# Kernel tuning notes

Hardware: AMD Instinct MI355X
Metric: run time of the kernel (lower is better)

The kernel has to match this reference:

```python
import jax, jax.numpy as jnp
import numpy as np

B, S, H = 2, 4096, 2048
NH, NKV, HD = 16, 4, 128          # heads, kv heads, head_dim = H // NH
GS_RATIO = 0.25                    # hardcoded in MyAttention.forward
ROPE_BASE = 10000.0


def rotate_half(x):
    h = x.shape[-1] // 2
    return jnp.concatenate((-x[..., h:], x[..., :h]), axis=-1)


def setup_inputs() -> dict:
    key = jax.random.key(0)
    ks = jax.random.split(key, 5)
    g = int(S * GS_RATIO)
    hidden_states = jax.random.normal(ks[0], (B, S, H), jnp.float32)
    position_ids = jnp.tile(jnp.arange(S, dtype=jnp.int32)[None, :], (B, 1))
    # causal additive mask per group window (0 keep, -1e9 masked)
    i = jnp.arange(g)
    causal = i[None, :] <= i[:, None]
    attention_mask = jnp.broadcast_to(
        jnp.where(causal, 0.0, -1e9).astype(jnp.float32)[None, None], (B, 1, g, g)
    )
    sc = 0.02
    Wq = (jax.random.normal(ks[1], (H, NH * HD), jnp.float32) * sc)
    Wk = (jax.random.normal(ks[2], (H, NKV * HD), jnp.float32) * sc)
    Wv = (jax.random.normal(ks[3], (H, NKV * HD), jnp.float32) * sc)
    Wo = (jax.random.normal(ks[4], (NH * HD, H), jnp.float32) * sc)
    return {"hidden_states": hidden_states, "attention_mask": attention_mask,
            "position_ids": position_ids, "Wq": Wq, "Wk": Wk, "Wv": Wv, "Wo": Wo}


def reference(hidden_states, attention_mask, position_ids, Wq, Wk, Wv, Wo):
    B_, S_, H_ = hidden_states.shape
    g = int(S_ * GS_RATIO)
    ng = S_ // g
    n_rep = NH // NKV

    # QKV projections -> (B, heads, S, HD)
    q = (hidden_states @ Wq).reshape(B_, S_, NH, HD).transpose(0, 2, 1, 3)
    k = (hidden_states @ Wk).reshape(B_, S_, NKV, HD).transpose(0, 2, 1, 3)
    v = (hidden_states @ Wv).reshape(B_, S_, NKV, HD).transpose(0, 2, 1, 3)

    # RoPE
    inv_freq = 1.0 / (ROPE_BASE ** (jnp.arange(0, HD, 2, dtype=jnp.float32) / HD))
    t = jnp.arange(S_, dtype=jnp.float32)
    emb = jnp.concatenate([jnp.outer(t, inv_freq)] * 2, axis=-1)  # (S, HD)
    cos = jnp.cos(emb)[position_ids][:, None]  # (B,1,S,HD)
    sin = jnp.sin(emb)[position_ids][:, None]
    q = q * cos + rotate_half(q) * sin
    k = k * cos + rotate_half(k) * sin

    # GQA repeat_kv
    k = jnp.repeat(k, n_rep, axis=1)
    v = jnp.repeat(v, n_rep, axis=1)

    # S2-Attn shift: roll second half of heads by -g/2 along seq, then group
    def shift(x):
        x = jnp.concatenate([x[:, :NH // 2],
                             jnp.roll(x[:, NH // 2:], -g // 2, axis=2)], axis=1)
        return x.transpose(0, 2, 1, 3).reshape(B_ * ng, g, NH, HD).transpose(0, 2, 1, 3)

    q, k, v = shift(q), shift(k), shift(v)

    attn = jnp.einsum('bhqd,bhkd->bhqk', q, k) / np.float32(np.sqrt(HD))
    mask = jnp.tile(attention_mask, (ng, 1, 1, 1))  # (B*ng,1,g,g)
    attn = attn + mask
    attn = jax.nn.softmax(attn.astype(jnp.float32), axis=-1).astype(q.dtype)

    out = jnp.einsum('bhqk,bhkd->bhqd', attn, v)  # (B*ng, NH, g, HD)
    out = out.transpose(0, 2, 1, 3).reshape(B_, S_, NH, HD)
    # undo shift for second half of heads (+g/2 along seq)
    out = jnp.concatenate([out[:, :, :NH // 2],
                           jnp.roll(out[:, :, NH // 2:], g // 2, axis=1)], axis=2)
    out = out.reshape(B_, S_, NH * HD) @ Wo
    return out
```

## Files before the change

kernel.cpp:

```cpp
#include <hip/hip_runtime.h>
#include <math.h>

typedef unsigned short u16;
typedef short bf16x8 __attribute__((ext_vector_type(8)));
typedef float f32x4 __attribute__((ext_vector_type(4)));


__device__ __forceinline__ u16 f2bf(float x) {
  union { float f; unsigned u; } c; c.f = x;
  unsigned r = (c.u + 0x7FFFu + ((c.u >> 16) & 1u)) >> 16;
  return (u16)r;
}
__device__ __forceinline__ float bf2f(u16 x) {
  union { unsigned u; float f; } c; c.u = ((unsigned)x) << 16;
  return c.f;
}

#define GLD16(gp, lp)                                                   \
  __builtin_amdgcn_global_load_lds(                                     \
      (__attribute__((address_space(1))) void*)(gp),                    \
      (__attribute__((address_space(3))) void*)(lp), 16, 0, 0)

__global__ __launch_bounds__(256) void cast_bf16_vec(
    const float* __restrict__ X, u16* __restrict__ Y) {
  const size_t i = ((size_t)blockIdx.x * 256 + threadIdx.x) * 4;
  float4 v = *(const float4*)(X + i);
  ushort4 o;
  o.x = f2bf(v.x); o.y = f2bf(v.y); o.z = f2bf(v.z); o.w = f2bf(v.w);
  *(ushort4*)(Y + i) = o;
}

__global__ __launch_bounds__(256) void wt_cast(
    const float* __restrict__ W, u16* __restrict__ Wt, int K, int N) {
  const int bk = blockIdx.y * 64;
  const int bn = blockIdx.x * 64;
  __shared__ float T[64 * 65];
  const int tid = threadIdx.x;
  #pragma unroll
  for (int u = 0; u < 16; ++u) {
    int idx = tid + u * 256;
    int kl = idx >> 6, nl = idx & 63;
    T[kl * 65 + nl] = W[(size_t)(bk + kl) * N + bn + nl];
  }
  __syncthreads();
  #pragma unroll
  for (int u = 0; u < 16; ++u) {
    int idx = tid + u * 256;
    int nl = idx >> 6, kl = idx & 63;
    Wt[(size_t)(bn + nl) * K + bk + kl] = f2bf(T[kl * 65 + nl]);
  }
}

__global__ __launch_bounds__(512) void gemm_bf16_256(
    const u16* __restrict__ A, const u16* __restrict__ Bt,
    float* __restrict__ Cf, u16* __restrict__ Cb, int M, int N, int K) {
  __shared__ u16 As[4][256 * 32];
  __shared__ u16 Bs[4][256 * 32];

  const int tid = threadIdx.x;

  const int gridN = N >> 8;
  const int nwg = gridDim.x * gridDim.y;
  const int orig = blockIdx.y * gridDim.x + blockIdx.x;
  const int q8 = nwg >> 3, r8 = nwg & 7;
  const int xcd = orig & 7, lid = orig >> 3;
  const int wgid = (xcd < r8 ? xcd * (q8 + 1) : r8 * (q8 + 1) + (xcd - r8) * q8) + lid;
  const int bm = (wgid / gridN) << 8;
  const int bn = (wgid % gridN) << 8;

  const int w = tid >> 6, lane = tid & 63;
  const int col = lane & 15, quad = lane >> 4;
  const int wm = w >> 2, wn = w & 3;
  const int sw = (col >> 1) & 3;

  const int srow = tid >> 2;
  const int scp  = tid & 3;
  const int sc   = scp ^ ((srow >> 1) & 3);

  const u16* Ag = A  + (size_t)bm * K;
  const u16* Bg = Bt + (size_t)bn * K;
  const u16* aS0 = Ag + (size_t)srow * K + sc * 8;
  const u16* aS1 = Ag + (size_t)(srow + 128) * K + sc * 8;
  const u16* bS0 = Bg + (size_t)srow * K + sc * 8;
  const u16* bS1 = Bg + (size_t)(srow + 128) * K + sc * 8;
  const int ldst0 = srow * 32 + scp * 8;
  const int ldst1 = (srow + 128) * 32 + scp * 8;

#define STAGE_A(t, buf) { GLD16(aS0 + (size_t)(t) * 32, &As[buf][ldst0]); \
                          GLD16(aS1 + (size_t)(t) * 32, &As[buf][ldst1]); }
#define STAGE_B(t, buf) { GLD16(bS0 + (size_t)(t) * 32, &Bs[buf][ldst0]); \
                          GLD16(bS1 + (size_t)(t) * 32, &Bs[buf][ldst1]); }

  f32x4 acc[8][4];
  #pragma unroll
  for (int i = 0; i < 8; ++i)
    #pragma unroll
    for (int j = 0; j < 4; ++j) acc[i][j] = (f32x4)(0.0f);

  const int NT = K >> 5;

  STAGE_A(0, 0); STAGE_B(0, 0);
  if (NT > 1) {
    STAGE_A(1, 1); STAGE_B(1, 1);
    asm volatile("s_waitcnt vmcnt(4)" ::: "memory");
  } else {
    asm volatile("s_waitcnt vmcnt(0)" ::: "memory");
  }
  __builtin_amdgcn_s_barrier();
  asm volatile("" ::: "memory");

  const int aoff = (wm * 128 + col) * 32 + (quad ^ sw) * 8;
  const int boff = (wn * 64  + col) * 32 + (quad ^ sw) * 8;

  for (int t = 0; t < NT; ++t) {
    const int cur = t & 3;
    const bool pf = (t + 2 < NT);
    const int pbuf = (t + 2) & 3;

    bf16x8 af[4], bfr[4];
    #pragma unroll
    for (int i = 0; i < 4; ++i)
      af[i] = *(const bf16x8*)&As[cur][aoff + (16 * i) * 32];
    #pragma unroll
    for (int j = 0; j < 4; ++j)
      bfr[j] = *(const bf16x8*)&Bs[cur][boff + (16 * j) * 32];
    if (pf) STAGE_A(t + 2, pbuf);
    __builtin_amdgcn_s_barrier();
    asm volatile("s_waitcnt lgkmcnt(0)");
    __builtin_amdgcn_s_setprio(1);
    #pragma unroll
    for (int i = 0; i < 4; ++i)
      #pragma unroll
      for (int j = 0; j < 4; ++j)
        acc[i][j] = __builtin_amdgcn_mfma_f32_16x16x32_bf16(af[i], bfr[j], acc[i][j], 0, 0, 0);
    __builtin_amdgcn_s_setprio(0);
    __builtin_amdgcn_s_barrier();

    bf16x8 af2[4];
    #pragma unroll
    for (int i = 0; i < 4; ++i)
      af2[i] = *(const bf16x8*)&As[cur][aoff + ((64 + 16 * i)) * 32];
    if (pf) STAGE_B(t + 2, pbuf);
    __builtin_amdgcn_s_barrier();
    asm volatile("s_waitcnt lgkmcnt(0)");
    __builtin_amdgcn_s_setprio(1);
    #pragma unroll
    for (int i = 0; i < 4; ++i)
      #pragma unroll
      for (int j = 0; j < 4; ++j)
        acc[4 + i][j] = __builtin_amdgcn_mfma_f32_16x16x32_bf16(af2[i], bfr[j], acc[4 + i][j], 0, 0, 0);
    __builtin_amdgcn_s_setprio(0);

    if (pf) asm volatile("s_waitcnt vmcnt(4)" ::: "memory");
    else    asm volatile("s_waitcnt vmcnt(0)" ::: "memory");
    __builtin_amdgcn_s_barrier();
    asm volatile("" ::: "memory");
  }

  const int crow0 = bm + wm * 128 + quad * 4;
  const int ccol0 = bn + wn * 64 + col;
  #pragma unroll
  for (int i = 0; i < 8; ++i) {
    const int row0 = crow0 + 16 * i;
    #pragma unroll
    for (int j = 0; j < 4; ++j) {
      const int cc = ccol0 + 16 * j;
      #pragma unroll
      for (int r = 0; r < 4; ++r) {
        if (Cb) Cb[(size_t)(row0 + r) * N + cc] = f2bf(acc[i][j][r]);
        else    Cf[(size_t)(row0 + r) * N + cc] = acc[i][j][r];
      }
    }
  }
#undef STAGE_A
#undef STAGE_B
}

__global__ __launch_bounds__(256) void rope_qkv(
    u16* __restrict__ QKV, const int* __restrict__ pos) {
  const unsigned idx = blockIdx.x * 256 + threadIdx.x;
  const int d = idx & 63;
  const unsigned rest = idx >> 6;
  const int hh = rest % 20;
  const unsigned bs = rest / 20;

  const int colbase = (hh < 16) ? hh * 128 : 2048 + (hh - 16) * 128;
  u16* p = QKV + (size_t)bs * 3072 + colbase + d;
  const float x0 = bf2f(p[0]);
  const float x1 = bf2f(p[64]);
  const float t = (float)pos[bs];
  const float inv_freq = __expf((float)d * -0.14391156509676332f);
  float s, c;
  __sincosf(t * inv_freq, &s, &c);
  const float sc = (hh < 16) ? 0.08838834764831845f : 1.0f;
  p[0]  = f2bf((x0 * c - x1 * s) * sc);
  p[64] = f2bf((x1 * c + x0 * s) * sc);
}

__global__ __launch_bounds__(256) void v_transpose(
    const u16* __restrict__ QKV, u16* __restrict__ Vt) {
  const int bid = blockIdx.x;
  const int st = bid & 63;
  const int kvh = (bid >> 6) & 3;
  const int b = bid >> 8;
  __shared__ u16 T[64 * 136];
  const int tid = threadIdx.x;
  #pragma unroll
  for (int u = 0; u < 4; ++u) {
    int idx = tid + u * 256;
    int sl = idx >> 4, ch = idx & 15;
    *(uint4*)&T[sl * 136 + ch * 8] =
        *(const uint4*)(QKV + ((size_t)(b * 4096 + st * 64 + sl)) * 3072 + 2560 + kvh * 128 + ch * 8);
  }
  __syncthreads();
  #pragma unroll
  for (int u = 0; u < 32; ++u) {
    int idx = tid + u * 256;
    int d = idx >> 6, sl = idx & 63;
    Vt[((size_t)((b * 4 + kvh) * 128 + d)) * 4096 + st * 64 + sl] = T[sl * 136 + d];
  }
}

__global__ __launch_bounds__(256) void attn_mfma(
    const u16* __restrict__ QKV, const u16* __restrict__ Vt,
    u16* __restrict__ Ob) {
  __shared__ u16 Ks[2][64 * 128];
  __shared__ u16 Vs[2][128 * 64];
  __shared__ u16 Ps[4][16 * 72];

  const int bid = blockIdx.x;
  const int qt = 15 - (bid & 15);
  const int h  = (bid >> 4) & 15;
  const int gi = (bid >> 8) & 3;
  const int b  = bid >> 10;

  const int tid = threadIdx.x;
  const int w = tid >> 6, lane = tid & 63;
  const int col = lane & 15, quad = lane >> 4;

  const int shift = (h >= 8) ? 512 : 0;
  const int base_s = gi * 1024;
  const int kvh = h >> 2;

  const int kco8 = ((tid & 15) ^ ((tid >> 4) & 7)) << 3;
  const int vco8 = ((tid & 7) ^ ((tid >> 3) & 7)) << 3;
  const size_t krow = (size_t)(tid >> 4) * 3072 + kco8;
  const size_t vrow = (size_t)(tid >> 3) * 4096 + vco8;
  u16* kdst = &Ks[0][0] + tid * 8;
  u16* vdst = &Vs[0][0] + tid * 8;
  const size_t vbase = (size_t)((b * 4 + kvh) * 128) * 4096;
  const u16* kgb = QKV + (size_t)b * 4096 * 3072 + 2048 + kvh * 128;

#define ASTAGE(kt_, buf_) {                                               \
    const int sk_ = (base_s + (kt_) * 64 + shift) & 4095;                 \
    const u16* ks_ = kgb + (size_t)sk_ * 3072;                            \
    const u16* vs_ = Vt + vbase + sk_;                                    \
    GLD16(ks_ + krow,             kdst + (buf_) * 8192);                  \
    GLD16(ks_ + krow + 16 * 3072, kdst + (buf_) * 8192 + 2048);           \
    GLD16(ks_ + krow + 32 * 3072, kdst + (buf_) * 8192 + 4096);           \
    GLD16(ks_ + krow + 48 * 3072, kdst + (buf_) * 8192 + 6144);           \
    GLD16(vs_ + vrow,             vdst + (buf_) * 8192);                  \
    GLD16(vs_ + vrow + 32 * 4096, vdst + (buf_) * 8192 + 2048);           \
    GLD16(vs_ + vrow + 64 * 4096, vdst + (buf_) * 8192 + 4096);           \
    GLD16(vs_ + vrow + 96 * 4096, vdst + (buf_) * 8192 + 6144);           \
  }

  const int sq0 = (base_s + qt * 64 + shift) & 4095;
  {
    const u16* qsrc = QKV + ((size_t)(b * 4096 + sq0)) * 3072 + h * 128;
    GLD16(qsrc + krow,             kdst);
    GLD16(qsrc + krow + 16 * 3072, kdst + 2048);
    GLD16(qsrc + krow + 32 * 3072, kdst + 4096);
    GLD16(qsrc + krow + 48 * 3072, kdst + 6144);
  }
  asm volatile("s_waitcnt vmcnt(0)" ::: "memory");
  __builtin_amdgcn_s_barrier();
  asm volatile("" ::: "memory");

  const int cxor = col & 7;
  bf16x8 aq[4];
  {
    const int qr = w * 16 + col;
    #pragma unroll
    for (int kk = 0; kk < 4; ++kk)
      aq[kk] = *(const bf16x8*)&Ks[0][qr * 128 + ((((kk << 2) + quad) ^ cxor) << 3)];
  }
  asm volatile("s_waitcnt lgkmcnt(0)" ::: "memory");
  __builtin_amdgcn_s_barrier();
  asm volatile("" ::: "memory");

  ASTAGE(0, 0);

  f32x4 o[8];
  #pragma unroll
  for (int jd = 0; jd < 8; ++jd) o[jd] = (f32x4)(0.0f);
  float lp[4] = {0.0f, 0.0f, 0.0f, 0.0f};

  u16* Pw = &Ps[w][0];
  const int qrow_l = w * 16 + quad * 4;

  for (int kt = 0; kt <= qt; ++kt) {
    const u16* Kc = &Ks[kt & 1][0];
    const u16* Vc = &Vs[kt & 1][0];
    const bool pf = (kt < qt);
    if (pf) ASTAGE(kt + 1, (kt + 1) & 1);
    if (pf) asm volatile("s_waitcnt vmcnt(8)" ::: "memory");
    else    asm volatile("s_waitcnt vmcnt(0)" ::: "memory");
    __builtin_amdgcn_s_barrier();
    asm volatile("" ::: "memory");

    f32x4 scv[4];
    #pragma unroll
    for (int j = 0; j < 4; ++j) scv[j] = (f32x4)(0.0f);
    __builtin_amdgcn_s_setprio(1);
    #pragma unroll
    for (int kk = 0; kk < 4; ++kk) {
      #pragma unroll
      for (int j = 0; j < 4; ++j) {
        bf16x8 bk = *(const bf16x8*)&Kc[(16 * j + col) * 128 + ((((kk << 2) + quad) ^ cxor) << 3)];
        scv[j] = __builtin_amdgcn_mfma_f32_16x16x32_bf16(aq[kk], bk, scv[j], 0, 0, 0);
      }
    }
    __builtin_amdgcn_s_setprio(0);

    const bool last = (kt == qt);
    #pragma unroll
    for (int j = 0; j < 4; ++j) {
      #pragma unroll
      for (int r = 0; r < 4; ++r) {
        float p = __expf(scv[j][r]);
        if (last && (16 * j + col) > (qrow_l + r)) p = 0.0f;
        lp[r] += p;
        Pw[(quad * 4 + r) * 72 + 16 * j + col] = f2bf(p);
      }
    }

    __builtin_amdgcn_s_setprio(1);
    #pragma unroll
    for (int ks = 0; ks < 2; ++ks) {
      bf16x8 ap = *(const bf16x8*)&Pw[col * 72 + ks * 32 + quad * 8];
      #pragma unroll
      for (int jd = 0; jd < 8; ++jd) {
        bf16x8 bv = *(const bf16x8*)&Vc[(16 * jd + col) * 64 + ((((ks << 2) + quad) ^ cxor) << 3)];
        o[jd] = __builtin_amdgcn_mfma_f32_16x16x32_bf16(ap, bv, o[jd], 0, 0, 0);
      }
    }
    __builtin_amdgcn_s_setprio(0);

    asm volatile("" ::: "memory");
    __builtin_amdgcn_s_barrier();
  }
#undef ASTAGE

  #pragma unroll
  for (int r = 0; r < 4; ++r) {
    lp[r] += __shfl_xor(lp[r], 1, 64);
    lp[r] += __shfl_xor(lp[r], 2, 64);
    lp[r] += __shfl_xor(lp[r], 4, 64);
    lp[r] += __shfl_xor(lp[r], 8, 64);
  }

  #pragma unroll
  for (int r = 0; r < 4; ++r) {
    const int qg = qt * 64 + w * 16 + quad * 4 + r;
    const int sq = (base_s + qg + shift) & 4095;
    u16* dst = Ob + ((size_t)(b * 4096 + sq)) * 2048 + h * 128;
    const float inv = 1.0f / lp[r];
    #pragma unroll
    for (int jd = 0; jd < 8; ++jd)
      dst[16 * jd + col] = f2bf(o[jd][r] * inv);
  }
}

extern "C" void kernel_launch(void* const* d_in, const int* in_sizes, int n_in,
                              void* d_out, int out_size, void* d_ws, size_t ws_size,
                              hipStream_t stream) {
  const float* hs = (const float*)d_in[0];
  const int*   pos = (const int*)d_in[2];
  const float* Wq = (const float*)d_in[3];
  const float* Wk = (const float*)d_in[4];
  const float* Wv = (const float*)d_in[5];
  const float* Wo = (const float*)d_in[6];

  char* ws = (char*)d_ws;
  u16* hsb   = (u16*)ws; ws += (size_t)8192 * 2048 * 2;
  u16* Wqkvt = (u16*)ws; ws += (size_t)3072 * 2048 * 2;
  u16* Wot   = (u16*)ws; ws += (size_t)2048 * 2048 * 2;
  u16* QKVb  = (u16*)ws; ws += (size_t)8192 * 3072 * 2;
  u16* Vtt   = (u16*)ws; ws += (size_t)2 * 4 * 128 * 4096 * 2;
  u16* Obh   = (u16*)ws; ws += (size_t)8192 * 2048 * 2;

  dim3 blk(256);

  cast_bf16_vec<<<16384, blk, 0, stream>>>(hs, hsb);
  wt_cast<<<dim3(32, 32), blk, 0, stream>>>(Wq, Wqkvt, 2048, 2048);
  wt_cast<<<dim3(8, 32),  blk, 0, stream>>>(Wk, Wqkvt + (size_t)2048 * 2048, 2048, 512);
  wt_cast<<<dim3(8, 32),  blk, 0, stream>>>(Wv, Wqkvt + (size_t)2560 * 2048, 2048, 512);
  wt_cast<<<dim3(32, 32), blk, 0, stream>>>(Wo, Wot, 2048, 2048);

  gemm_bf16_256<<<dim3(12, 32), dim3(512), 0, stream>>>(hsb, Wqkvt, nullptr, QKVb, 8192, 3072, 2048);

  rope_qkv<<<40960, blk, 0, stream>>>(QKVb, pos);

  v_transpose<<<512, blk, 0, stream>>>(QKVb, Vtt);

  attn_mfma<<<2048, blk, 0, stream>>>(QKVb, Vtt, Obh);

  gemm_bf16_256<<<dim3(8, 32), dim3(512), 0, stream>>>(Obh, Wot, (float*)d_out, nullptr, 8192, 2048, 2048);
}
```

Measured before the change: 502.6 us.

## Deepen GEMM prefetch to three stages and add 256x192 tile QKV GEMM

The generic bf16 GEMM now prefetches three k-tiles ahead into its four LDS buffers instead of two, with vmcnt waits adjusted to match. A new specialized QKV projection kernel uses 256x192 output tiles, giving 512 workgroups (two per CU on 256 CUs) instead of 384, to balance the wave count across CUs. It also uses the deeper prefetch, with a per-thread-half vmcnt accounting because only half the threads issue the second B load. The risks are more LDS traffic and pressure, plus subtle waitcnt correctness.

```diff
diff --git a/kernel.cpp b/kernel.cpp
--- a/kernel.cpp
+++ b/kernel.cpp
@@ -100,12 +100,11 @@
   const int NT = K >> 5;
 
   STAGE_A(0, 0); STAGE_B(0, 0);
-  if (NT > 1) {
-    STAGE_A(1, 1); STAGE_B(1, 1);
-    asm volatile("s_waitcnt vmcnt(4)" ::: "memory");
-  } else {
-    asm volatile("s_waitcnt vmcnt(0)" ::: "memory");
-  }
+  if (NT > 1) { STAGE_A(1, 1); STAGE_B(1, 1); }
+  if (NT > 2) { STAGE_A(2, 2); STAGE_B(2, 2); }
+  if (NT > 2)      asm volatile("s_waitcnt vmcnt(8)" ::: "memory");
+  else if (NT > 1) asm volatile("s_waitcnt vmcnt(4)" ::: "memory");
+  else             asm volatile("s_waitcnt vmcnt(0)" ::: "memory");
   __builtin_amdgcn_s_barrier();
   asm volatile("" ::: "memory");
 
@@ -114,8 +113,8 @@
 
   for (int t = 0; t < NT; ++t) {
     const int cur = t & 3;
-    const bool pf = (t + 2 < NT);
-    const int pbuf = (t + 2) & 3;
+    const bool pf = (t + 3 < NT);
+    const int pbuf = (t + 3) & 3;
 
     bf16x8 af[4], bfr[4];
     #pragma unroll
@@ -124,7 +123,7 @@
     #pragma unroll
     for (int j = 0; j < 4; ++j)
       bfr[j] = *(const bf16x8*)&Bs[cur][boff + (16 * j) * 32];
-    if (pf) STAGE_A(t + 2, pbuf);
+    if (pf) STAGE_A(t + 3, pbuf);
     __builtin_amdgcn_s_barrier();
     asm volatile("s_waitcnt lgkmcnt(0)");
     __builtin_amdgcn_s_setprio(1);
@@ -140,7 +139,7 @@
     #pragma unroll
     for (int i = 0; i < 4; ++i)
       af2[i] = *(const bf16x8*)&As[cur][aoff + ((64 + 16 * i)) * 32];
-    if (pf) STAGE_B(t + 2, pbuf);
+    if (pf) STAGE_B(t + 3, pbuf);
     __builtin_amdgcn_s_barrier();
     asm volatile("s_waitcnt lgkmcnt(0)");
     __builtin_amdgcn_s_setprio(1);
@@ -151,8 +150,10 @@
         acc[4 + i][j] = __builtin_amdgcn_mfma_f32_16x16x32_bf16(af2[i], bfr[j], acc[4 + i][j], 0, 0, 0);
     __builtin_amdgcn_s_setprio(0);
 
-    if (pf) asm volatile("s_waitcnt vmcnt(4)" ::: "memory");
-    else    asm volatile("s_waitcnt vmcnt(0)" ::: "memory");
+    const int rem = NT - 1 - t;
+    if (rem >= 3)      asm volatile("s_waitcnt vmcnt(8)" ::: "memory");
+    else if (rem == 2) asm volatile("s_waitcnt vmcnt(4)" ::: "memory");
+    else if (rem == 1) asm volatile("s_waitcnt vmcnt(0)" ::: "memory");
     __builtin_amdgcn_s_barrier();
     asm volatile("" ::: "memory");
   }
@@ -174,6 +175,126 @@
   }
 #undef STAGE_A
 #undef STAGE_B
+}
+
+__global__ __launch_bounds__(512) void gemm_qkv_192(
+    const u16* __restrict__ A, const u16* __restrict__ Bt,
+    u16* __restrict__ Cb) {
+  const int K = 2048, N = 3072, NT = 64;
+  __shared__ u16 As[4][256 * 32];
+  __shared__ u16 Bs[4][192 * 32];
+
+  const int tid = threadIdx.x;
+
+  const int orig = blockIdx.y * gridDim.x + blockIdx.x;
+  const int wgid = (orig & 7) * 64 + (orig >> 3);
+  const int bm = (wgid >> 4) << 8;
+  const int bn = (wgid & 15) * 192;
+
+  const int w = tid >> 6, lane = tid & 63;
+  const int col = lane & 15, quad = lane >> 4;
+  const int wm = w >> 2, wn = w & 3;
+  const int sw = (col >> 1) & 3;
+
+  const int srow = tid >> 2;
+  const int scp  = tid & 3;
+  const int sc   = scp ^ ((srow >> 1) & 3);
+
+  const u16* Ag = A  + (size_t)bm * K;
+  const u16* Bg = Bt + (size_t)bn * K;
+  const u16* aS0 = Ag + (size_t)srow * K + sc * 8;
+  const u16* aS1 = Ag + (size_t)(srow + 128) * K + sc * 8;
+  const u16* bS0 = Bg + (size_t)srow * K + sc * 8;
+  const u16* bS1 = Bg + (size_t)(srow + 128) * K + sc * 8;
+  const int ldst0 = srow * 32 + scp * 8;
+  const int ldst1 = (srow + 128) * 32 + scp * 8;
+
+#define STAGEQ(t, buf) {                                                  \
+    GLD16(aS0 + (size_t)(t) * 32, &As[buf][ldst0]);                       \
+    GLD16(aS1 + (size_t)(t) * 32, &As[buf][ldst1]);                       \
+    GLD16(bS0 + (size_t)(t) * 32, &Bs[buf][ldst0]);                       \
+    if (tid < 256) GLD16(bS1 + (size_t)(t) * 32, &Bs[buf][ldst1]);        \
+  }
+
+  f32x4 acc[8][3];
+  #pragma unroll
+  for (int i = 0; i < 8; ++i)
+    #pragma unroll
+    for (int j = 0; j < 3; ++j) acc[i][j] = (f32x4)(0.0f);
+
+  STAGEQ(0, 0); STAGEQ(1, 1); STAGEQ(2, 2);
+  if (tid < 256) asm volatile("s_waitcnt vmcnt(8)" ::: "memory");
+  else           asm volatile("s_waitcnt vmcnt(6)" ::: "memory");
+  __builtin_amdgcn_s_barrier();
+  asm volatile("" ::: "memory");
+
+  const int aoff = (wm * 128 + col) * 32 + (quad ^ sw) * 8;
+  const int boff = (wn * 48  + col) * 32 + (quad ^ sw) * 8;
+
+  for (int t = 0; t < NT; ++t) {
+    const int cur = t & 3;
+    if (t + 3 < NT) STAGEQ(t + 3, (t + 3) & 3);
+
+    bf16x8 af[4], bfr[3];
+    #pragma unroll
+    for (int i = 0; i < 4; ++i)
+      af[i] = *(const bf16x8*)&As[cur][aoff + (16 * i) * 32];
+    #pragma unroll
+    for (int j = 0; j < 3; ++j)
+      bfr[j] = *(const bf16x8*)&Bs[cur][boff + (16 * j) * 32];
+    __builtin_amdgcn_s_barrier();
+    asm volatile("s_waitcnt lgkmcnt(0)");
+    __builtin_amdgcn_s_setprio(1);
+    #pragma unroll
+    for (int i = 0; i < 4; ++i)
+      #pragma unroll
+      for (int j = 0; j < 3; ++j)
+        acc[i][j] = __builtin_amdgcn_mfma_f32_16x16x32_bf16(af[i], bfr[j], acc[i][j], 0, 0, 0);
+    __builtin_amdgcn_s_setprio(0);
+    __builtin_amdgcn_s_barrier();
+
+    bf16x8 af2[4];
+    #pragma unroll
+    for (int i = 0; i < 4; ++i)
+      af2[i] = *(const bf16x8*)&As[cur][aoff + ((64 + 16 * i)) * 32];
+    __builtin_amdgcn_s_barrier();
+    asm volatile("s_waitcnt lgkmcnt(0)");
+    __builtin_amdgcn_s_setprio(1);
+    #pragma unroll
+    for (int i = 0; i < 4; ++i)
+      #pragma unroll
+      for (int j = 0; j < 3; ++j)
+        acc[4 + i][j] = __builtin_amdgcn_mfma_f32_16x16x32_bf16(af2[i], bfr[j], acc[4 + i][j], 0, 0, 0);
+    __builtin_amdgcn_s_setprio(0);
+
+    const int rem = NT - 1 - t;
+    if (rem >= 3) {
+      if (tid < 256) asm volatile("s_waitcnt vmcnt(8)" ::: "memory");
+      else           asm volatile("s_waitcnt vmcnt(6)" ::: "memory");
+    } else if (rem == 2) {
+      if (tid < 256) asm volatile("s_waitcnt vmcnt(4)" ::: "memory");
+      else           asm volatile("s_waitcnt vmcnt(3)" ::: "memory");
+    } else if (rem == 1) {
+      asm volatile("s_waitcnt vmcnt(0)" ::: "memory");
+    }
+    __builtin_amdgcn_s_barrier();
+    asm volatile("" ::: "memory");
+  }
+
+  const int crow0 = bm + wm * 128 + quad * 4;
+  const int ccol0 = bn + wn * 48 + col;
+  #pragma unroll
+  for (int i = 0; i < 8; ++i) {
+    const int row0 = crow0 + 16 * i;
+    #pragma unroll
+    for (int j = 0; j < 3; ++j) {
+      const int cc = ccol0 + 16 * j;
+      #pragma unroll
+      for (int r = 0; r < 4; ++r)
+        Cb[(size_t)(row0 + r) * N + cc] = f2bf(acc[i][j][r]);
+    }
+  }
+#undef STAGEQ
 }
 
 __global__ __launch_bounds__(256) void rope_qkv(
@@ -398,7 +519,7 @@
   wt_cast<<<dim3(8, 32),  blk, 0, stream>>>(Wv, Wqkvt + (size_t)2560 * 2048, 2048, 512);
   wt_cast<<<dim3(32, 32), blk, 0, stream>>>(Wo, Wot, 2048, 2048);
 
-  gemm_bf16_256<<<dim3(12, 32), dim3(512), 0, stream>>>(hsb, Wqkvt, nullptr, QKVb, 8192, 3072, 2048);
+  gemm_qkv_192<<<dim3(16, 32), dim3(512), 0, stream>>>(hsb, Wqkvt, QKVb);
 
   rope_qkv<<<40960, blk, 0, stream>>>(QKVb, pos);
 
```

Result: slower. 528.7 us (+5.2%).

## Restructure GEMM to double-buffered pipeline and use 256x128 tiles for output projection

Applied to the files above, without the earlier changes.

Replaces the 4-buffer split-phase GEMM pipeline with a templated double-buffered kernel. It loads all A/B fragments at once, runs a single MFMA block, then prefetches into the freed buffer. LDS use is halved to allow more waves per CU. The output projection now uses 256x128 tiles, giving 512 workgroups instead of 256 for better CU fill on the 2048-wide GEMM. The cost is less overlap of global loads with MFMA and more register pressure from holding 8 A fragments. The XCD remap is simplified and assumes the workgroup count divides by 8.

```diff
diff --git a/kernel.cpp b/kernel.cpp
--- a/kernel.cpp
+++ b/kernel.cpp
@@ -20,6 +20,8 @@
   __builtin_amdgcn_global_load_lds(                                     \
       (__attribute__((address_space(1))) void*)(gp),                    \
       (__attribute__((address_space(3))) void*)(lp), 16, 0, 0)
+
+#define WAITVM(n) asm volatile("s_waitcnt vmcnt(" #n ")" ::: "memory")
 
 __global__ __launch_bounds__(256) void cast_bf16_vec(
     const float* __restrict__ X, u16* __restrict__ Y) {
@@ -51,22 +53,25 @@
   }
 }
 
-__global__ __launch_bounds__(512) void gemm_bf16_256(
+template <int BN>
+__global__ __launch_bounds__(512, 4) void gemm_db(
     const u16* __restrict__ A, const u16* __restrict__ Bt,
     float* __restrict__ Cf, u16* __restrict__ Cb, int M, int N, int K) {
-  __shared__ u16 As[4][256 * 32];
-  __shared__ u16 Bs[4][256 * 32];
+  constexpr int NJ = BN / 64;
+  constexpr int LB = BN / 128;
+
+  __shared__ u16 As[2][256 * 32];
+  __shared__ u16 Bs[2][BN * 32];
 
   const int tid = threadIdx.x;
 
-  const int gridN = N >> 8;
+  const int gridN = N / BN;
   const int nwg = gridDim.x * gridDim.y;
   const int orig = blockIdx.y * gridDim.x + blockIdx.x;
-  const int q8 = nwg >> 3, r8 = nwg & 7;
-  const int xcd = orig & 7, lid = orig >> 3;
-  const int wgid = (xcd < r8 ? xcd * (q8 + 1) : r8 * (q8 + 1) + (xcd - r8) * q8) + lid;
+  const int q8 = nwg >> 3;
+  const int wgid = (orig & 7) * q8 + (orig >> 3);
   const int bm = (wgid / gridN) << 8;
-  const int bn = (wgid % gridN) << 8;
+  const int bn = (wgid % gridN) * BN;
 
   const int w = tid >> 6, lane = tid & 63;
   const int col = lane & 15, quad = lane >> 4;
@@ -77,93 +82,77 @@
   const int scp  = tid & 3;
   const int sc   = scp ^ ((srow >> 1) & 3);
 
-  const u16* Ag = A  + (size_t)bm * K;
-  const u16* Bg = Bt + (size_t)bn * K;
-  const u16* aS0 = Ag + (size_t)srow * K + sc * 8;
-  const u16* aS1 = Ag + (size_t)(srow + 128) * K + sc * 8;
-  const u16* bS0 = Bg + (size_t)srow * K + sc * 8;
-  const u16* bS1 = Bg + (size_t)(srow + 128) * K + sc * 8;
+  const u16* aS0 = A  + (size_t)(bm + srow) * K + sc * 8;
+  const u16* aS1 = A  + (size_t)(bm + srow + 128) * K + sc * 8;
+  const u16* bS0 = Bt + (size_t)(bn + srow) * K + sc * 8;
+  const u16* bS1 = Bt + (size_t)(bn + srow + 128) * K + sc * 8;
   const int ldst0 = srow * 32 + scp * 8;
   const int ldst1 = (srow + 128) * 32 + scp * 8;
 
-#define STAGE_A(t, buf) { GLD16(aS0 + (size_t)(t) * 32, &As[buf][ldst0]); \
-                          GLD16(aS1 + (size_t)(t) * 32, &As[buf][ldst1]); }
-#define STAGE_B(t, buf) { GLD16(bS0 + (size_t)(t) * 32, &Bs[buf][ldst0]); \
-                          GLD16(bS1 + (size_t)(t) * 32, &Bs[buf][ldst1]); }
-
-  f32x4 acc[8][4];
+#define STAGE(t, buf) {                                                   \
+    GLD16(aS0 + (size_t)(t) * 32, &As[buf][ldst0]);                       \
+    GLD16(aS1 + (size_t)(t) * 32, &As[buf][ldst1]);                       \
+    GLD16(bS0 + (size_t)(t) * 32, &Bs[buf][ldst0]);                       \
+    if constexpr (LB == 2) GLD16(bS1 + (size_t)(t) * 32, &Bs[buf][ldst1]); \
+  }
+
+  f32x4 acc[8][NJ];
   #pragma unroll
   for (int i = 0; i < 8; ++i)
     #pragma unroll
-    for (int j = 0; j < 4; ++j) acc[i][j] = (f32x4)(0.0f);
+    for (int j = 0; j < NJ; ++j) acc[i][j] = (f32x4)(0.0f);
 
   const int NT = K >> 5;
 
-  STAGE_A(0, 0); STAGE_B(0, 0);
-  if (NT > 1) {
-    STAGE_A(1, 1); STAGE_B(1, 1);
-    asm volatile("s_waitcnt vmcnt(4)" ::: "memory");
-  } else {
-    asm volatile("s_waitcnt vmcnt(0)" ::: "memory");
-  }
+  STAGE(0, 0); STAGE(1, 1);
+  if constexpr (LB == 2) WAITVM(4); else WAITVM(3);
   __builtin_amdgcn_s_barrier();
   asm volatile("" ::: "memory");
 
   const int aoff = (wm * 128 + col) * 32 + (quad ^ sw) * 8;
-  const int boff = (wn * 64  + col) * 32 + (quad ^ sw) * 8;
+  const int boff = (wn * (BN / 4) + col) * 32 + (quad ^ sw) * 8;
 
   for (int t = 0; t < NT; ++t) {
-    const int cur = t & 3;
-    const bool pf = (t + 2 < NT);
-    const int pbuf = (t + 2) & 3;
-
-    bf16x8 af[4], bfr[4];
-    #pragma unroll
-    for (int i = 0; i < 4; ++i)
+    const int cur = t & 1;
+
+    bf16x8 af[8], bfr[NJ];
+    #pragma unroll
+    for (int i = 0; i < 8; ++i)
       af[i] = *(const bf16x8*)&As[cur][aoff + (16 * i) * 32];
     #pragma unroll
-    for (int j = 0; j < 4; ++j)
+    for (int j = 0; j < NJ; ++j)
       bfr[j] = *(const bf16x8*)&Bs[cur][boff + (16 * j) * 32];
-    if (pf) STAGE_A(t + 2, pbuf);
-    __builtin_amdgcn_s_barrier();
-    asm volatile("s_waitcnt lgkmcnt(0)");
+
     __builtin_amdgcn_s_setprio(1);
     #pragma unroll
-    for (int i = 0; i < 4; ++i)
-      #pragma unroll
-      for (int j = 0; j < 4; ++j)
+    for (int i = 0; i < 8; ++i)
+      #pragma unroll
+      for (int j = 0; j < NJ; ++j)
         acc[i][j] = __builtin_amdgcn_mfma_f32_16x16x32_bf16(af[i], bfr[j], acc[i][j], 0, 0, 0);
     __builtin_amdgcn_s_setprio(0);
+
+    asm volatile("" ::: "memory");
     __builtin_amdgcn_s_barrier();
 
-    bf16x8 af2[4];
-    #pragma unroll
-    for (int i = 0; i < 4; ++i)
-      af2[i] = *(const bf16x8*)&As[cur][aoff + ((64 + 16 * i)) * 32];
-    if (pf) STAGE_B(t + 2, pbuf);
-    __builtin_amdgcn_s_barrier();
-    asm volatile("s_waitcnt lgkmcnt(0)");
-    __builtin_amdgcn_s_setprio(1);
-    #pragma unroll
-    for (int i = 0; i < 4; ++i)
-      #pragma unroll
-      for (int j = 0; j < 4; ++j)
-        acc[4 + i][j] = __builtin_amdgcn_mfma_f32_16x16x32_bf16(af2[i], bfr[j], acc[4 + i][j], 0, 0, 0);
-    __builtin_amdgcn_s_setprio(0);
-
-    if (pf) asm volatile("s_waitcnt vmcnt(4)" ::: "memory");
-    else    asm volatile("s_waitcnt vmcnt(0)" ::: "memory");
-    __builtin_amdgcn_s_barrier();
-    asm volatile("" ::: "memory");
+    if (t + 2 < NT) {
+      STAGE(t + 2, cur);
+      if constexpr (LB == 2) WAITVM(4); else WAITVM(3);
+      __builtin_amdgcn_s_barrier();
+      asm volatile("" ::: "memory");
+    } else if (t + 1 < NT) {
+      WAITVM(0);
+      __builtin_amdgcn_s_barrier();
+      asm volatile("" ::: "memory");
+    }
   }
 
   const int crow0 = bm + wm * 128 + quad * 4;
-  const int ccol0 = bn + wn * 64 + col;
+  const int ccol0 = bn + wn * (BN / 4) + col;
   #pragma unroll
   for (int i = 0; i < 8; ++i) {
     const int row0 = crow0 + 16 * i;
     #pragma unroll
-    for (int j = 0; j < 4; ++j) {
+    for (int j = 0; j < NJ; ++j) {
       const int cc = ccol0 + 16 * j;
       #pragma unroll
       for (int r = 0; r < 4; ++r) {
@@ -172,8 +161,7 @@
       }
     }
   }
-#undef STAGE_A
-#undef STAGE_B
+#undef STAGE
 }
 
 __global__ __launch_bounds__(256) void rope_qkv(
@@ -398,7 +386,7 @@
   wt_cast<<<dim3(8, 32),  blk, 0, stream>>>(Wv, Wqkvt + (size_t)2560 * 2048, 2048, 512);
   wt_cast<<<dim3(32, 32), blk, 0, stream>>>(Wo, Wot, 2048, 2048);
 
-  gemm_bf16_256<<<dim3(12, 32), dim3(512), 0, stream>>>(hsb, Wqkvt, nullptr, QKVb, 8192, 3072, 2048);
+  gemm_db<256><<<dim3(12, 32), dim3(512), 0, stream>>>(hsb, Wqkvt, nullptr, QKVb, 8192, 3072, 2048);
 
   rope_qkv<<<40960, blk, 0, stream>>>(QKVb, pos);
 
@@ -406,5 +394,5 @@
 
   attn_mfma<<<2048, blk, 0, stream>>>(QKVb, Vtt, Obh);
 
-  gemm_bf16_256<<<dim3(8, 32), dim3(512), 0, stream>>>(Obh, Wot, (float*)d_out, nullptr, 8192, 2048, 2048);
-}
+  gemm_db<128><<<dim3(16, 32), dim3(512), 0, stream>>>(Obh, Wot, (float*)d_out, nullptr, 8192, 2048, 2048);
+}
```

New measurement: 1.456 ms. +189.7%, slower.
